# Kernel optimization log

Hardware: AMD Instinct MI355X
Metric: run time of the kernel (lower is better)

## Reference

```python
import jax, jax.numpy as jnp
import numpy as np

D_MODEL = 1024
N_HEADS = 16
SCALES = (1, 2, 4, 8)
B, S = 4, 2048
NS = len(SCALES)
E = D_MODEL // NS        # per-scale embed dim = 256
H = N_HEADS // NS        # per-scale heads = 4
DK = E // H              # head dim = 64


def setup_inputs() -> dict:
    key = jax.random.key(0)
    ks = jax.random.split(key, 6)
    sc = lambda fan_in: 1.0 / np.sqrt(fan_in)
    return {
        "x": jax.random.normal(ks[0], (B, S, D_MODEL), jnp.float32),
        # per-scale projection Linear(d_model -> E), stacked over scales
        "proj_W": jax.random.normal(ks[1], (NS, D_MODEL, E), jnp.float32) * sc(D_MODEL),
        "proj_b": jnp.zeros((NS, E), jnp.float32),
        # per-scale MultiheadAttention in_proj (q,k,v packed) and out_proj
        "in_W": jax.random.normal(ks[2], (NS, E, 3 * E), jnp.float32) * sc(E),
        "in_b": jnp.zeros((NS, 3 * E), jnp.float32),
        "out_W": jax.random.normal(ks[3], (NS, E, E), jnp.float32) * sc(E),
        "out_b": jnp.zeros((NS, E), jnp.float32),
        # fusion: Linear(d_model -> d_model) + LayerNorm (dropout is identity in eval)
        "fus_W": jax.random.normal(ks[4], (D_MODEL, D_MODEL), jnp.float32) * sc(D_MODEL),
        "fus_b": jnp.zeros((D_MODEL,), jnp.float32),
        "ln_g": jnp.ones((D_MODEL,), jnp.float32),
        "ln_b": jnp.zeros((D_MODEL,), jnp.float32),
    }


def _mha(x, in_W, in_b, out_W, out_b):
    # torch nn.MultiheadAttention, batch_first, eval mode, need_weights=True
    b, L, _ = x.shape
    qkv = x @ in_W + in_b                       # [b, L, 3E]
    q, k, v = jnp.split(qkv, 3, axis=-1)
    heads = lambda t: t.reshape(b, L, H, DK).transpose(0, 2, 1, 3)  # [b,h,L,dk]
    q, k, v = heads(q), heads(k), heads(v)
    scores = jnp.einsum('bhqd,bhkd->bhqk', q, k) / np.sqrt(DK).astype(np.float32)
    probs = jax.nn.softmax(scores, axis=-1)
    o = jnp.einsum('bhqk,bhkd->bhqd', probs, v).transpose(0, 2, 1, 3).reshape(b, L, E)
    return o @ out_W + out_b, probs.mean(axis=1)  # averaged over heads: [b,L,L]


def _upsample(y, s):
    # Faithful vectorization of the torch interpolation loop when S % s == 0:
    # full[k*s + j] = (1 - j/s)*y[k] + (j/s)*y[k+1], with zero right-neighbor
    # for the last block (torch reads attn_out_full[S-1] while it is still 0).
    if s == 1:
        return y
    b, K, d = y.shape
    y_next = jnp.concatenate([y[:, 1:], jnp.zeros_like(y[:, :1])], axis=1)
    alpha = (jnp.arange(s, dtype=y.dtype) / s)[None, None, :, None]  # [1,1,s,1]
    full = (1.0 - alpha) * y[:, :, None, :] + alpha * y_next[:, :, None, :]
    return full.reshape(b, K * s, d)


def reference(x, proj_W, proj_b, in_W, in_b, out_W, out_b, fus_W, fus_b, ln_g, ln_b):
    scale_outputs = []
    w0 = None
    for i, s in enumerate(SCALES):
        x_scale = x @ proj_W[i] + proj_b[i]        # [B,S,E]
        x_sub = x_scale[:, ::s, :]                 # strided subsequence [B,S//s,E]
        y, w = _mha(x_sub, in_W[i], in_b[i], out_W[i], out_b[i])
        scale_outputs.append(_upsample(y, s))
        if i == 0:
            w0 = w                                  # combined_weights = first scale's weights
    z = jnp.concatenate(scale_outputs, axis=-1) @ fus_W + fus_b
    mu = z.mean(-1, keepdims=True)
    var = z.var(-1, keepdims=True)
    fused = (z - mu) / jnp.sqrt(var + 1e-5) * ln_g + ln_b
    return fused, w0
```

## Files before the change

### kernel.cpp

```cpp
#include <hip/hip_runtime.h>
#include <hip/hip_bf16.h>


typedef short bh8 __attribute__((ext_vector_type(8)));
typedef float f32x4 __attribute__((ext_vector_type(4)));

#define CLOG2E 0.18033688011112042f

__device__ __forceinline__ ushort f2b(float f) {
    __hip_bfloat16 h = __float2bfloat16(f);
    return *reinterpret_cast<ushort*>(&h);
}
__device__ __forceinline__ float b2f(ushort u) {
    __hip_bfloat16 h;
    *reinterpret_cast<ushort*>(&h) = u;
    return __bfloat162float(h);
}
__device__ __forceinline__ float fexp2(float x) {
    float r;
    asm("v_exp_f32 %0, %1" : "=v"(r) : "v"(x));
    return r;
}
template<int CTRL>
__device__ __forceinline__ float dpp_mv(float x) {
    int i = __float_as_int(x);
    int r = __builtin_amdgcn_update_dpp(i, i, CTRL, 0xF, 0xF, false);
    return __int_as_float(r);
}
__device__ __forceinline__ float row_max16(float t) {
    t = fmaxf(t, dpp_mv<0x128>(t));
    t = fmaxf(t, dpp_mv<0x124>(t));
    t = fmaxf(t, dpp_mv<0x122>(t));
    t = fmaxf(t, dpp_mv<0x121>(t));
    return t;
}
__device__ __forceinline__ float row_sum16(float t) {
    t += dpp_mv<0x128>(t);
    t += dpp_mv<0x124>(t);
    t += dpp_mv<0x122>(t);
    t += dpp_mv<0x121>(t);
    return t;
}

__global__ __launch_bounds__(256) void cvt_kernel(
    const float* __restrict__ s, ushort* __restrict__ d, long n)
{
    long i = ((long)blockIdx.x * 256 + threadIdx.x) * 4;
    if (i >= n) return;
    float4 v = *(const float4*)(s + i);
    ushort4 o;
    o.x = f2b(v.x); o.y = f2b(v.y); o.z = f2b(v.z); o.w = f2b(v.w);
    *(ushort4*)(d + i) = o;
}

__global__ __launch_bounds__(256) void wtrans_kernel(
    const float* __restrict__ src, ushort* __restrict__ dst, int K, int N)
{
    __shared__ float Ls[32][33];
    const int n0 = blockIdx.x * 32, k0 = blockIdx.y * 32;
    const float* s = src + (long)blockIdx.z * K * N;
    ushort* d = dst + (long)blockIdx.z * N * K;
    const int tid = threadIdx.x;
    #pragma unroll
    for (int it = 0; it < 4; ++it) {
        int f = tid + it * 256;
        int kc = f >> 5, rn = f & 31;
        Ls[kc][rn] = s[(long)(k0 + kc) * N + n0 + rn];
    }
    __syncthreads();
    #pragma unroll
    for (int it = 0; it < 2; ++it) {
        int f = tid + it * 256;
        int rn = f >> 4, kc2 = (f & 15) * 2;
        ushort2 o;
        o.x = f2b(Ls[kc2][rn]);
        o.y = f2b(Ls[kc2 + 1][rn]);
        *(ushort2*)&d[(long)(n0 + rn) * K + k0 + kc2] = o;
    }
}

template<int MODE>
__global__ __launch_bounds__(256) void gemm_ms(
    const ushort* __restrict__ A, const ushort* __restrict__ Wt,
    const float* __restrict__ bias, ushort* __restrict__ C)
{
    constexpr int K = (MODE == 0) ? 1024 : 256;
    constexpr int N = (MODE == 1) ? 768 : 256;
    __shared__ ushort As[128][72];
    __shared__ ushort Bs[128][72];

    const int tid = threadIdx.x;
    const int wave = tid >> 6, lane = tid & 63;
    const int lm = lane & 15, quad = lane >> 4;
    const int wm = (wave & 1) * 64, wn = (wave >> 1) * 64;
    const int m0 = blockIdx.x * 128, n0 = blockIdx.y * 128;
    const int s = (m0 >= 14336) ? 3 : ((m0 >= 12288) ? 2 : ((m0 >= 8192) ? 1 : 0));
    const ushort* Wp = Wt + (long)s * N * K;
    const float* bp_ = bias + s * N;

    f32x4 acc[4][4];
    #pragma unroll
    for (int i = 0; i < 4; ++i)
        #pragma unroll
        for (int j = 0; j < 4; ++j) {
            f32x4 zz = {0.f, 0.f, 0.f, 0.f};
            acc[i][j] = zz;
        }

    const int r0 = tid >> 3, k8 = (tid & 7) * 8;
    const ushort* ap[4];
    #pragma unroll
    for (int it = 0; it < 4; ++it) {
        int m = m0 + r0 + it * 32;
        if (MODE == 0) {
            int t = m - (16384 - (16384 >> s));
            int b = t >> (11 - s);
            int tt = t - (b << (11 - s));
            ap[it] = A + ((long)(b * 2048) + ((long)tt << s)) * 1024 + k8;
        } else {
            ap[it] = A + (long)m * K + k8;
        }
    }
    const ushort* bp[4];
    #pragma unroll
    for (int it = 0; it < 4; ++it)
        bp[it] = Wp + (long)(n0 + r0 + it * 32) * K + k8;

    for (int k0 = 0; k0 < K; k0 += 64) {
        #pragma unroll
        for (int it = 0; it < 4; ++it)
            *(bh8*)&As[r0 + it * 32][k8] = *(const bh8*)(ap[it] + k0);
        #pragma unroll
        for (int it = 0; it < 4; ++it)
            *(bh8*)&Bs[r0 + it * 32][k8] = *(const bh8*)(bp[it] + k0);
        __syncthreads();
        #pragma unroll
        for (int ks = 0; ks < 2; ++ks) {
            bh8 af[4], bfv[4];
            #pragma unroll
            for (int i = 0; i < 4; ++i)
                af[i] = *(const bh8*)&As[wm + i * 16 + lm][ks * 32 + quad * 8];
            #pragma unroll
            for (int j = 0; j < 4; ++j)
                bfv[j] = *(const bh8*)&Bs[wn + j * 16 + lm][ks * 32 + quad * 8];
            #pragma unroll
            for (int i = 0; i < 4; ++i)
                #pragma unroll
                for (int j = 0; j < 4; ++j)
                    acc[i][j] = __builtin_amdgcn_mfma_f32_16x16x32_bf16(
                        af[i], bfv[j], acc[i][j], 0, 0, 0);
        }
        __syncthreads();
    }

    float bv[4]; int cols[4];
    #pragma unroll
    for (int j = 0; j < 4; ++j) {
        cols[j] = n0 + wn + j * 16 + lm;
        bv[j] = bp_[cols[j]];
    }
    #pragma unroll
    for (int i = 0; i < 4; ++i) {
        int mb = m0 + wm + i * 16 + quad * 4;
        #pragma unroll
        for (int j = 0; j < 4; ++j)
            #pragma unroll
            for (int r = 0; r < 4; ++r)
                C[(long)(mb + r) * N + cols[j]] = f2b(acc[i][j][r] + bv[j]);
    }
}

__global__ __launch_bounds__(256) void vtrans_ms(
    const ushort* __restrict__ qkvb, ushort* __restrict__ vTb)
{
    __shared__ ushort Ls[64][72];
    const int bid = blockIdx.x;
    const int s = (bid >= 896) ? 3 : ((bid >= 768) ? 2 : ((bid >= 512) ? 1 : 0));
    const int rel = bid - ((s == 0) ? 0 : ((s == 1) ? 512 : ((s == 2) ? 768 : 896)));
    const int L = 2048 >> s;
    const int z = rel >> (5 - s);
    const int kt = rel & ((32 >> s) - 1);
    const int b = z >> 2, h = z & 3;
    const ushort* src = qkvb + (long)(16384 - (16384 >> s)) * 768
                        + (long)b * L * 768 + 512 + h * 64;
    const int k0 = kt * 64;
    const int tid = threadIdx.x;
    const int kk = tid >> 3, d8 = (tid & 7) * 8;
    #pragma unroll
    for (int it = 0; it < 2; ++it) {
        int k = kk + it * 32;
        bh8 v = *(const bh8*)(src + (long)(k0 + k) * 768 + d8);
        ushort tmp[8];
        *(bh8*)tmp = v;
        #pragma unroll
        for (int j = 0; j < 8; ++j) Ls[d8 + j][k] = tmp[j];
    }
    __syncthreads();
    ushort* dst = vTb + (long)(4096 - (4096 >> s)) * 1024 + (long)z * 64 * L;
    #pragma unroll
    for (int it = 0; it < 2; ++it) {
        int d = kk + it * 32;
        *(bh8*)(dst + (long)d * L + k0 + d8) = *(const bh8*)&Ls[d][d8];
    }
}

__global__ __launch_bounds__(256, 3) void attn_ms(
    const ushort* __restrict__ qkvb, const ushort* __restrict__ vTb,
    ushort* __restrict__ ob, float* __restrict__ msc, float* __restrict__ invl)
{
    __shared__ ushort Ks[128 * 72];
    __shared__ ushort Vs[64 * 136];
    __shared__ ushort Ps[64 * 136];

    const int bid = blockIdx.x;
    const int s = (bid >= 896) ? 3 : ((bid >= 768) ? 2 : ((bid >= 512) ? 1 : 0));
    const int rel = bid - ((s == 0) ? 0 : ((s == 1) ? 512 : ((s == 2) ? 768 : 896)));
    const int L = 2048 >> s;
    const int z = rel >> (5 - s);
    const int qt = rel & ((32 >> s) - 1);
    const int b = z >> 2, h = z & 3;
    const int Rr16 = 16384 - (16384 >> s);
    const ushort* qbase = qkvb + (long)Rr16 * 768 + (long)b * L * 768 + h * 64;
    const ushort* kbase = qbase + 256;
    const ushort* vbase = vTb + (long)(4096 - (4096 >> s)) * 1024 + (long)z * 64 * L;
    ushort* o = ob + (long)Rr16 * 256;

    const int tid = threadIdx.x;
    const int wave = tid >> 6, lane = tid & 63;
    const int lm = lane & 15, quad = lane >> 4;
    const int wm = wave * 16;
    const int q0 = qt * 64;
    const int r0 = tid >> 3, k8 = (tid & 7) * 8;
    const int vd0 = tid >> 4, vc8 = (tid & 15) * 8;

    #pragma unroll
    for (int it = 0; it < 2; ++it) {
        int row = r0 + it * 32;
        *(bh8*)&Ps[row * 136 + k8] = *(const bh8*)(qbase + (long)(q0 + row) * 768 + k8);
    }
    bh8 kreg[4], vreg[4];
    #pragma unroll
    for (int it = 0; it < 4; ++it)
        kreg[it] = *(const bh8*)(kbase + (long)(r0 + it * 32) * 768 + k8);
    #pragma unroll
    for (int it = 0; it < 4; ++it)
        vreg[it] = *(const bh8*)(vbase + (long)(vd0 + it * 16) * L + vc8);
    #pragma unroll
    for (int it = 0; it < 4; ++it)
        *(bh8*)&Ks[(r0 + it * 32) * 72 + k8] = kreg[it];
    #pragma unroll
    for (int it = 0; it < 4; ++it)
        *(bh8*)&Vs[(vd0 + it * 16) * 136 + vc8] = vreg[it];
    __syncthreads();

    bh8 qf[2];
    #pragma unroll
    for (int ks = 0; ks < 2; ++ks)
        qf[ks] = *(const bh8*)&Ps[(wm + lm) * 136 + ks * 32 + quad * 8];

    f32x4 oc[4];
    #pragma unroll
    for (int nj = 0; nj < 4; ++nj) {
        f32x4 zz = {0.f, 0.f, 0.f, 0.f};
        oc[nj] = zz;
    }
    float mh[4], l_run[4];
    #pragma unroll
    for (int rr = 0; rr < 4; ++rr) { mh[rr] = -3.0e38f; l_run[rr] = 0.f; }

    for (int k0 = 0; k0 < L; k0 += 128) {
        const int kn = k0 + 128;
        const bool hasnext = kn < L;
        if (hasnext) {
            #pragma unroll
            for (int it = 0; it < 4; ++it)
                kreg[it] = *(const bh8*)(kbase + (long)(kn + r0 + it * 32) * 768 + k8);
            #pragma unroll
            for (int it = 0; it < 4; ++it)
                vreg[it] = *(const bh8*)(vbase + (long)(vd0 + it * 16) * L + kn + vc8);
        }

        f32x4 sc[8];
        #pragma unroll
        for (int nj = 0; nj < 8; ++nj) {
            f32x4 zz = {0.f, 0.f, 0.f, 0.f};
            sc[nj] = zz;
        }
        __builtin_amdgcn_s_setprio(1);
        #pragma unroll
        for (int ks = 0; ks < 2; ++ks)
            #pragma unroll
            for (int nj = 0; nj < 8; ++nj) {
                bh8 kf = *(const bh8*)&Ks[(nj * 16 + lm) * 72 + ks * 32 + quad * 8];
                sc[nj] = __builtin_amdgcn_mfma_f32_16x16x32_bf16(qf[ks], kf, sc[nj], 0, 0, 0);
            }
        __builtin_amdgcn_s_setprio(0);

        #pragma unroll
        for (int rr = 0; rr < 4; ++rr) {
            float t01 = fmaxf(sc[0][rr], sc[1][rr]);
            float t23 = fmaxf(sc[2][rr], sc[3][rr]);
            float t45 = fmaxf(sc[4][rr], sc[5][rr]);
            float t67 = fmaxf(sc[6][rr], sc[7][rr]);
            float t = fmaxf(fmaxf(t01, t23), fmaxf(t45, t67));
            t = row_max16(t);
            float mo = mh[rr];
            float mn = fmaxf(mo, t * CLOG2E);
            float alpha = fexp2(mo - mn);
            mh[rr] = mn;
            int prow = (wm + quad * 4 + rr) * 136;
            float p[8];
            #pragma unroll
            for (int nj = 0; nj < 8; ++nj) {
                p[nj] = fexp2(fmaf(sc[nj][rr], CLOG2E, -mn));
                Ps[prow + nj * 16 + lm] = f2b(p[nj]);
            }
            float rs = ((p[0] + p[1]) + (p[2] + p[3])) + ((p[4] + p[5]) + (p[6] + p[7]));
            rs = row_sum16(rs);
            l_run[rr] = l_run[rr] * alpha + rs;
            #pragma unroll
            for (int nj = 0; nj < 4; ++nj) oc[nj][rr] *= alpha;
        }

        __builtin_amdgcn_s_setprio(1);
        #pragma unroll
        for (int kst = 0; kst < 4; ++kst) {
            bh8 pf = *(const bh8*)&Ps[(wm + lm) * 136 + kst * 32 + quad * 8];
            #pragma unroll
            for (int nj = 0; nj < 4; ++nj) {
                bh8 vf = *(const bh8*)&Vs[(nj * 16 + lm) * 136 + kst * 32 + quad * 8];
                oc[nj] = __builtin_amdgcn_mfma_f32_16x16x32_bf16(pf, vf, oc[nj], 0, 0, 0);
            }
        }
        __builtin_amdgcn_s_setprio(0);

        __syncthreads();
        if (hasnext) {
            #pragma unroll
            for (int it = 0; it < 4; ++it)
                *(bh8*)&Ks[(r0 + it * 32) * 72 + k8] = kreg[it];
            #pragma unroll
            for (int it = 0; it < 4; ++it)
                *(bh8*)&Vs[(vd0 + it * 16) * 136 + vc8] = vreg[it];
            __syncthreads();
        }
    }

    #pragma unroll
    for (int rr = 0; rr < 4; ++rr) {
        float il = 1.f / l_run[rr];
        int q = q0 + wm + quad * 4 + rr;
        if (s == 0 && lm == 0) {
            msc[z * 2048 + q] = mh[rr];
            invl[z * 2048 + q] = il;
        }
        long rbase = ((long)(b * L + q)) * 256 + h * 64;
        #pragma unroll
        for (int nj = 0; nj < 4; ++nj)
            o[rbase + nj * 16 + lm] = f2b(oc[nj][rr] * il);
    }
}

__global__ __launch_bounds__(256, 2) void w0_recompute(
    const ushort* __restrict__ qkv,
    const float* __restrict__ msc, const float* __restrict__ invl,
    float* __restrict__ w0)
{
    const int L = 2048;
    __shared__ ushort SH[18432];
    ushort* Qs = SH;
    ushort* Ks = SH + 9216;
    ushort* Ws = SH;

    const int tid = threadIdx.x;
    const int wave = tid >> 6, lane = tid & 63;
    const int lm = lane & 15, quad = lane >> 4;
    const int wm = wave * 32;
    const int q0 = blockIdx.x * 128, k0 = blockIdx.y * 128;
    const int b = blockIdx.z;
    const int r0 = tid >> 3, k8 = (tid & 7) * 8;

    f32x4 acc[2][8];
    #pragma unroll
    for (int mi = 0; mi < 2; ++mi)
        #pragma unroll
        for (int nj = 0; nj < 8; ++nj) {
            f32x4 zz = {0.f, 0.f, 0.f, 0.f};
            acc[mi][nj] = zz;
        }

    for (int h = 0; h < 4; ++h) {
        const ushort* qb = qkv + (long)b * L * 768 + h * 64;
        const ushort* kb = qb + 256;
        #pragma unroll
        for (int it = 0; it < 4; ++it) {
            int r = r0 + it * 32;
            *(bh8*)&Qs[r * 72 + k8] = *(const bh8*)(qb + (long)(q0 + r) * 768 + k8);
            *(bh8*)&Ks[r * 72 + k8] = *(const bh8*)(kb + (long)(k0 + r) * 768 + k8);
        }
        __syncthreads();
        bh8 qf[2][2];
        #pragma unroll
        for (int mi = 0; mi < 2; ++mi)
            #pragma unroll
            for (int ks = 0; ks < 2; ++ks)
                qf[mi][ks] = *(const bh8*)&Qs[(wm + mi * 16 + lm) * 72 + ks * 32 + quad * 8];
        f32x4 sc[2][8];
        #pragma unroll
        for (int mi = 0; mi < 2; ++mi)
            #pragma unroll
            for (int nj = 0; nj < 8; ++nj) {
                f32x4 zz = {0.f, 0.f, 0.f, 0.f};
                sc[mi][nj] = zz;
            }
        #pragma unroll
        for (int ks = 0; ks < 2; ++ks)
            #pragma unroll
            for (int nj = 0; nj < 8; ++nj) {
                bh8 kf = *(const bh8*)&Ks[(nj * 16 + lm) * 72 + ks * 32 + quad * 8];
                #pragma unroll
                for (int mi = 0; mi < 2; ++mi)
                    sc[mi][nj] = __builtin_amdgcn_mfma_f32_16x16x32_bf16(
                        qf[mi][ks], kf, sc[mi][nj], 0, 0, 0);
            }
        const float* mz = msc + (long)(b * 4 + h) * L;
        const float* iz = invl + (long)(b * 4 + h) * L;
        #pragma unroll
        for (int mi = 0; mi < 2; ++mi)
            #pragma unroll
            for (int rr = 0; rr < 4; ++rr) {
                int q = q0 + wm + mi * 16 + quad * 4 + rr;
                float mv = mz[q], iv = iz[q];
                #pragma unroll
                for (int nj = 0; nj < 8; ++nj)
                    acc[mi][nj][rr] += fexp2(fmaf(sc[mi][nj][rr], CLOG2E, -mv)) * iv;
            }
        __syncthreads();
    }

    #pragma unroll
    for (int mi = 0; mi < 2; ++mi)
        #pragma unroll
        for (int rr = 0; rr < 4; ++rr) {
            int prow = (wm + mi * 16 + quad * 4 + rr) * 136;
            #pragma unroll
            for (int nj = 0; nj < 8; ++nj)
                Ws[prow + nj * 16 + lm] = f2b(0.25f * acc[mi][nj][rr]);
        }
    __syncthreads();
    #pragma unroll
    for (int it = 0; it < 8; ++it) {
        int idx = tid + it * 256;
        int row = idx >> 4, c8 = (idx & 15) * 8;
        ushort tmp[8];
        *(bh8*)tmp = *(const bh8*)&Ws[row * 136 + c8];
        long base = ((long)b * 2048 + q0 + row) * 2048 + k0 + c8;
        float4 f0, f1;
        f0.x = b2f(tmp[0]); f0.y = b2f(tmp[1]); f0.z = b2f(tmp[2]); f0.w = b2f(tmp[3]);
        f1.x = b2f(tmp[4]); f1.y = b2f(tmp[5]); f1.z = b2f(tmp[6]); f1.w = b2f(tmp[7]);
        *(float4*)&w0[base] = f0;
        *(float4*)&w0[base + 4] = f1;
    }
}

__global__ __launch_bounds__(256) void upsample_ms(
    const ushort* __restrict__ yallb, ushort* __restrict__ ccat)
{
    const int bid = blockIdx.x;
    const int s = bid >> 11;
    const int idx = (bid & 2047) * 256 + threadIdx.x;
    const int c4 = (idx & 63) * 4;
    const int t = (idx >> 6) & 2047;
    const int b = idx >> 17;
    const int L = 2048 >> s;
    const int k = t >> s, j = t & ((1 << s) - 1);
    const float a = (float)j / (float)(1 << s);
    const ushort* y = yallb + (long)(16384 - (16384 >> s)) * 256;
    const ushort* y0p = y + ((long)(b * L + k)) * 256 + c4;
    ushort4 y0 = *(const ushort4*)y0p;
    ushort4 y1 = {0, 0, 0, 0};
    if (k + 1 < L) y1 = *(const ushort4*)(y0p + 256);
    ushort4 o;
    o.x = f2b((1.f - a) * b2f(y0.x) + a * b2f(y1.x));
    o.y = f2b((1.f - a) * b2f(y0.y) + a * b2f(y1.y));
    o.z = f2b((1.f - a) * b2f(y0.z) + a * b2f(y1.z));
    o.w = f2b((1.f - a) * b2f(y0.w) + a * b2f(y1.w));
    *(ushort4*)&ccat[((long)(b * 2048 + t)) * 1024 + s * 256 + c4] = o;
}

__global__ __launch_bounds__(256) void gemm_fus(
    const ushort* __restrict__ A, const ushort* __restrict__ Wt,
    const float* __restrict__ bias, float* __restrict__ C)
{
    const int K = 1024, N = 1024;
    __shared__ ushort As[128][72];
    __shared__ ushort Bs[128][72];
    const int tid = threadIdx.x;
    const int wave = tid >> 6, lane = tid & 63;
    const int lm = lane & 15, quad = lane >> 4;
    const int wm = (wave & 1) * 64, wn = (wave >> 1) * 64;
    const int m0 = blockIdx.x * 128, n0 = blockIdx.y * 128;

    f32x4 acc[4][4];
    #pragma unroll
    for (int i = 0; i < 4; ++i)
        #pragma unroll
        for (int j = 0; j < 4; ++j) {
            f32x4 zz = {0.f, 0.f, 0.f, 0.f};
            acc[i][j] = zz;
        }
    const int r0 = tid >> 3, k8 = (tid & 7) * 8;
    for (int k0 = 0; k0 < K; k0 += 64) {
        #pragma unroll
        for (int it = 0; it < 4; ++it) {
            int r = r0 + it * 32;
            *(bh8*)&As[r][k8] = *(const bh8*)(A + (long)(m0 + r) * K + k0 + k8);
            *(bh8*)&Bs[r][k8] = *(const bh8*)(Wt + (long)(n0 + r) * K + k0 + k8);
        }
        __syncthreads();
        #pragma unroll
        for (int ks = 0; ks < 2; ++ks) {
            bh8 af[4], bfv[4];
            #pragma unroll
            for (int i = 0; i < 4; ++i)
                af[i] = *(const bh8*)&As[wm + i * 16 + lm][ks * 32 + quad * 8];
            #pragma unroll
            for (int j = 0; j < 4; ++j)
                bfv[j] = *(const bh8*)&Bs[wn + j * 16 + lm][ks * 32 + quad * 8];
            #pragma unroll
            for (int i = 0; i < 4; ++i)
                #pragma unroll
                for (int j = 0; j < 4; ++j)
                    acc[i][j] = __builtin_amdgcn_mfma_f32_16x16x32_bf16(
                        af[i], bfv[j], acc[i][j], 0, 0, 0);
        }
        __syncthreads();
    }
    float bv[4]; int cols[4];
    #pragma unroll
    for (int j = 0; j < 4; ++j) {
        cols[j] = n0 + wn + j * 16 + lm;
        bv[j] = bias[cols[j]];
    }
    #pragma unroll
    for (int i = 0; i < 4; ++i) {
        int mb = m0 + wm + i * 16 + quad * 4;
        #pragma unroll
        for (int j = 0; j < 4; ++j)
            #pragma unroll
            for (int r = 0; r < 4; ++r)
                C[(long)(mb + r) * N + cols[j]] = acc[i][j][r] + bv[j];
    }
}

__global__ __launch_bounds__(256) void ln_kernel(
    float* __restrict__ zbuf, const float* __restrict__ g, const float* __restrict__ bta)
{
    long row = blockIdx.x;
    float* p = zbuf + row * 1024;
    const int tid = threadIdx.x;
    float4 v = *(const float4*)(p + tid * 4);
    float s = (v.x + v.y) + (v.z + v.w);
    #pragma unroll
    for (int off = 32; off; off >>= 1) s += __shfl_xor(s, off);
    __shared__ float r0[4], r1[4];
    int wid = tid >> 6;
    if ((tid & 63) == 0) r0[wid] = s;
    __syncthreads();
    s = r0[0] + r0[1] + r0[2] + r0[3];
    float mu = s * (1.f / 1024.f);
    float dx = v.x - mu, dy = v.y - mu, dz = v.z - mu, dw = v.w - mu;
    float q = (dx * dx + dy * dy) + (dz * dz + dw * dw);
    #pragma unroll
    for (int off = 32; off; off >>= 1) q += __shfl_xor(q, off);
    if ((tid & 63) == 0) r1[wid] = q;
    __syncthreads();
    q = r1[0] + r1[1] + r1[2] + r1[3];
    float rstd = rsqrtf(q * (1.f / 1024.f) + 1e-5f);
    float4 gg = *(const float4*)(g + tid * 4);
    float4 bb = *(const float4*)(bta + tid * 4);
    float4 o;
    o.x = dx * rstd * gg.x + bb.x;
    o.y = dy * rstd * gg.y + bb.y;
    o.z = dz * rstd * gg.z + bb.z;
    o.w = dw * rstd * gg.w + bb.w;
    *(float4*)(p + tid * 4) = o;
}

extern "C" void kernel_launch(void* const* d_in, const int* in_sizes, int n_in,
                              void* d_out, int out_size, void* d_ws, size_t ws_size,
                              hipStream_t stream)
{
    const float* x     = (const float*)d_in[0];
    const float* projW = (const float*)d_in[1];
    const float* projB = (const float*)d_in[2];
    const float* inW   = (const float*)d_in[3];
    const float* inB   = (const float*)d_in[4];
    const float* outW  = (const float*)d_in[5];
    const float* outB  = (const float*)d_in[6];
    const float* fusW  = (const float*)d_in[7];
    const float* fusB  = (const float*)d_in[8];
    const float* lnG   = (const float*)d_in[9];
    const float* lnB   = (const float*)d_in[10];

    float* fused  = (float*)d_out;
    float* out_w0 = fused + 8388608;

    char* w = (char*)d_ws;
    ushort* xb     = (ushort*)w; w += 16777216;
    ushort* pT     = (ushort*)w; w += 2097152;
    ushort* iT     = (ushort*)w; w += 1572864;
    ushort* oT     = (ushort*)w; w += 524288;
    ushort* fT     = (ushort*)w; w += 2097152;
    ushort* xprojb = (ushort*)w; w += 7864320;
    ushort* qkvb   = (ushort*)w; w += 23592960;
    ushort* ob     = (ushort*)w; w += 7864320;
    ushort* yallb  = (ushort*)w; w += 7864320;
    ushort* ccatb  = (ushort*)w; w += 16777216;
    ushort* vTb    = (ushort*)w; w += 7864320;
    float*  msc    = (float*)w;  w += 131072;
    float*  invl   = (float*)w;  w += 131072;

    cvt_kernel<<<8192, 256, 0, stream>>>(x, xb, 8388608);
    wtrans_kernel<<<dim3(8, 32, 4), 256, 0, stream>>>(projW, pT, 1024, 256);
    wtrans_kernel<<<dim3(24, 8, 4), 256, 0, stream>>>(inW, iT, 256, 768);
    wtrans_kernel<<<dim3(8, 8, 4), 256, 0, stream>>>(outW, oT, 256, 256);
    wtrans_kernel<<<dim3(32, 32, 1), 256, 0, stream>>>(fusW, fT, 1024, 1024);

    gemm_ms<0><<<dim3(120, 2), 256, 0, stream>>>(xb, pT, projB, xprojb);
    gemm_ms<1><<<dim3(120, 6), 256, 0, stream>>>(xprojb, iT, inB, qkvb);
    vtrans_ms<<<960, 256, 0, stream>>>(qkvb, vTb);
    attn_ms<<<960, 256, 0, stream>>>(qkvb, vTb, ob, msc, invl);
    w0_recompute<<<dim3(16, 16, 4), 256, 0, stream>>>(qkvb, msc, invl, out_w0);
    gemm_ms<2><<<dim3(120, 2), 256, 0, stream>>>(ob, oT, outB, yallb);
    upsample_ms<<<8192, 256, 0, stream>>>(yallb, ccatb);
    gemm_fus<<<dim3(64, 8), 256, 0, stream>>>(ccatb, fT, fusB, fused);
    ln_kernel<<<8192, 256, 0, stream>>>(fused, lnG, lnB);
}
```

Baseline: 340.1 us.

## Fuse prep kernels, prefetch GEMM tiles into registers, shrink BM for small GEMMs

Merges the input-convert and four weight-transpose launches into one prep kernel to cut launch overhead. Adds register prefetch of the next K-tile in the GEMMs, fusion GEMM and the w0 recompute Q/K loads, so global loads overlap MFMA work, and raises wave priority around MFMA blocks. Halves the M tile to 64 for the projection and out-proj GEMMs, doubling grid size to fill more CUs. This costs more registers, an extra barrier per iteration, and more B-tile reloads in the smaller-tile GEMMs.

```diff
diff --git a/kernel.cpp b/kernel.cpp
--- a/kernel.cpp
+++ b/kernel.cpp
@@ -42,25 +42,13 @@
     return t;
 }
 
-__global__ __launch_bounds__(256) void cvt_kernel(
-    const float* __restrict__ s, ushort* __restrict__ d, long n)
-{
-    long i = ((long)blockIdx.x * 256 + threadIdx.x) * 4;
-    if (i >= n) return;
-    float4 v = *(const float4*)(s + i);
-    ushort4 o;
-    o.x = f2b(v.x); o.y = f2b(v.y); o.z = f2b(v.z); o.w = f2b(v.w);
-    *(ushort4*)(d + i) = o;
-}
-
-__global__ __launch_bounds__(256) void wtrans_kernel(
-    const float* __restrict__ src, ushort* __restrict__ dst, int K, int N)
-{
-    __shared__ float Ls[32][33];
-    const int n0 = blockIdx.x * 32, k0 = blockIdx.y * 32;
-    const float* s = src + (long)blockIdx.z * K * N;
-    ushort* d = dst + (long)blockIdx.z * N * K;
-    const int tid = threadIdx.x;
+__device__ __forceinline__ void wtrans_body(
+    const float* __restrict__ src, ushort* __restrict__ dst,
+    int K, int N, int bx, int by, int z, int tid, float (*Ls)[33])
+{
+    const int n0 = bx * 32, k0 = by * 32;
+    const float* s = src + (long)z * K * N;
+    ushort* d = dst + (long)z * N * K;
     #pragma unroll
     for (int it = 0; it < 4; ++it) {
         int f = tid + it * 256;
@@ -79,6 +67,40 @@
     }
 }
 
+__global__ __launch_bounds__(256) void prep_kernel(
+    const float* __restrict__ x, ushort* __restrict__ xb,
+    const float* __restrict__ projW, ushort* __restrict__ pT,
+    const float* __restrict__ inW, ushort* __restrict__ iT,
+    const float* __restrict__ outW, ushort* __restrict__ oT,
+    const float* __restrict__ fusW, ushort* __restrict__ fT)
+{
+    __shared__ float Ls[32][33];
+    const int bid = blockIdx.x;
+    const int tid = threadIdx.x;
+    if (bid < 8192) {
+        long i = ((long)bid * 256 + tid) * 4;
+        float4 v = *(const float4*)(x + i);
+        ushort4 o;
+        o.x = f2b(v.x); o.y = f2b(v.y); o.z = f2b(v.z); o.w = f2b(v.w);
+        *(ushort4*)(xb + i) = o;
+    } else if (bid < 9216) {
+        int rel = bid - 8192;
+        int z = rel >> 8, rem = rel & 255;
+        wtrans_body(projW, pT, 1024, 256, rem & 7, rem >> 3, z, tid, Ls);
+    } else if (bid < 9984) {
+        int rel = bid - 9216;
+        int z = rel / 192, rem = rel - z * 192;
+        wtrans_body(inW, iT, 256, 768, rem % 24, rem / 24, z, tid, Ls);
+    } else if (bid < 10240) {
+        int rel = bid - 9984;
+        int z = rel >> 6, rem = rel & 63;
+        wtrans_body(outW, oT, 256, 256, rem & 7, rem >> 3, z, tid, Ls);
+    } else {
+        int rel = bid - 10240;
+        wtrans_body(fusW, fT, 1024, 1024, rel & 31, rel >> 5, 0, tid, Ls);
+    }
+}
+
 template<int MODE>
 __global__ __launch_bounds__(256) void gemm_ms(
     const ushort* __restrict__ A, const ushort* __restrict__ Wt,
@@ -86,21 +108,24 @@
 {
     constexpr int K = (MODE == 0) ? 1024 : 256;
     constexpr int N = (MODE == 1) ? 768 : 256;
-    __shared__ ushort As[128][72];
+    constexpr int BM = (MODE == 1) ? 128 : 64;
+    constexpr int MF = BM / 32;
+    constexpr int AITS = BM / 32;
+    __shared__ ushort As[BM][72];
     __shared__ ushort Bs[128][72];
 
     const int tid = threadIdx.x;
     const int wave = tid >> 6, lane = tid & 63;
     const int lm = lane & 15, quad = lane >> 4;
-    const int wm = (wave & 1) * 64, wn = (wave >> 1) * 64;
-    const int m0 = blockIdx.x * 128, n0 = blockIdx.y * 128;
+    const int wm = (wave & 1) * (BM / 2), wn = (wave >> 1) * 64;
+    const int m0 = blockIdx.x * BM, n0 = blockIdx.y * 128;
     const int s = (m0 >= 14336) ? 3 : ((m0 >= 12288) ? 2 : ((m0 >= 8192) ? 1 : 0));
     const ushort* Wp = Wt + (long)s * N * K;
     const float* bp_ = bias + s * N;
 
-    f32x4 acc[4][4];
-    #pragma unroll
-    for (int i = 0; i < 4; ++i)
+    f32x4 acc[MF][4];
+    #pragma unroll
+    for (int i = 0; i < MF; ++i)
         #pragma unroll
         for (int j = 0; j < 4; ++j) {
             f32x4 zz = {0.f, 0.f, 0.f, 0.f};
@@ -108,9 +133,9 @@
         }
 
     const int r0 = tid >> 3, k8 = (tid & 7) * 8;
-    const ushort* ap[4];
-    #pragma unroll
-    for (int it = 0; it < 4; ++it) {
+    const ushort* ap[AITS];
+    #pragma unroll
+    for (int it = 0; it < AITS; ++it) {
         int m = m0 + r0 + it * 32;
         if (MODE == 0) {
             int t = m - (16384 - (16384 >> s));
@@ -126,31 +151,52 @@
     for (int it = 0; it < 4; ++it)
         bp[it] = Wp + (long)(n0 + r0 + it * 32) * K + k8;
 
+    bh8 areg[AITS], breg[4];
+    #pragma unroll
+    for (int it = 0; it < AITS; ++it) areg[it] = *(const bh8*)(ap[it]);
+    #pragma unroll
+    for (int it = 0; it < 4; ++it) breg[it] = *(const bh8*)(bp[it]);
+    #pragma unroll
+    for (int it = 0; it < AITS; ++it) *(bh8*)&As[r0 + it * 32][k8] = areg[it];
+    #pragma unroll
+    for (int it = 0; it < 4; ++it) *(bh8*)&Bs[r0 + it * 32][k8] = breg[it];
+    __syncthreads();
+
     for (int k0 = 0; k0 < K; k0 += 64) {
-        #pragma unroll
-        for (int it = 0; it < 4; ++it)
-            *(bh8*)&As[r0 + it * 32][k8] = *(const bh8*)(ap[it] + k0);
-        #pragma unroll
-        for (int it = 0; it < 4; ++it)
-            *(bh8*)&Bs[r0 + it * 32][k8] = *(const bh8*)(bp[it] + k0);
-        __syncthreads();
+        const int kn = k0 + 64;
+        const bool hasnext = kn < K;
+        if (hasnext) {
+            #pragma unroll
+            for (int it = 0; it < AITS; ++it) areg[it] = *(const bh8*)(ap[it] + kn);
+            #pragma unroll
+            for (int it = 0; it < 4; ++it) breg[it] = *(const bh8*)(bp[it] + kn);
+        }
+        __builtin_amdgcn_s_setprio(1);
         #pragma unroll
         for (int ks = 0; ks < 2; ++ks) {
-            bh8 af[4], bfv[4];
-            #pragma unroll
-            for (int i = 0; i < 4; ++i)
+            bh8 af[MF], bfv[4];
+            #pragma unroll
+            for (int i = 0; i < MF; ++i)
                 af[i] = *(const bh8*)&As[wm + i * 16 + lm][ks * 32 + quad * 8];
             #pragma unroll
             for (int j = 0; j < 4; ++j)
                 bfv[j] = *(const bh8*)&Bs[wn + j * 16 + lm][ks * 32 + quad * 8];
             #pragma unroll
-            for (int i = 0; i < 4; ++i)
+            for (int i = 0; i < MF; ++i)
                 #pragma unroll
                 for (int j = 0; j < 4; ++j)
                     acc[i][j] = __builtin_amdgcn_mfma_f32_16x16x32_bf16(
                         af[i], bfv[j], acc[i][j], 0, 0, 0);
         }
+        __builtin_amdgcn_s_setprio(0);
         __syncthreads();
+        if (hasnext) {
+            #pragma unroll
+            for (int it = 0; it < AITS; ++it) *(bh8*)&As[r0 + it * 32][k8] = areg[it];
+            #pragma unroll
+            for (int it = 0; it < 4; ++it) *(bh8*)&Bs[r0 + it * 32][k8] = breg[it];
+            __syncthreads();
+        }
     }
 
     float bv[4]; int cols[4];
@@ -160,7 +206,7 @@
         bv[j] = bp_[cols[j]];
     }
     #pragma unroll
-    for (int i = 0; i < 4; ++i) {
+    for (int i = 0; i < MF; ++i) {
         int mb = m0 + wm + i * 16 + quad * 4;
         #pragma unroll
         for (int j = 0; j < 4; ++j)
@@ -389,16 +435,36 @@
             acc[mi][nj] = zz;
         }
 
-    for (int h = 0; h < 4; ++h) {
-        const ushort* qb = qkv + (long)b * L * 768 + h * 64;
+    bh8 qreg[4], kreg[4];
+    {
+        const ushort* qb = qkv + (long)b * L * 768;
         const ushort* kb = qb + 256;
         #pragma unroll
         for (int it = 0; it < 4; ++it) {
             int r = r0 + it * 32;
-            *(bh8*)&Qs[r * 72 + k8] = *(const bh8*)(qb + (long)(q0 + r) * 768 + k8);
-            *(bh8*)&Ks[r * 72 + k8] = *(const bh8*)(kb + (long)(k0 + r) * 768 + k8);
+            qreg[it] = *(const bh8*)(qb + (long)(q0 + r) * 768 + k8);
+            kreg[it] = *(const bh8*)(kb + (long)(k0 + r) * 768 + k8);
+        }
+    }
+
+    for (int h = 0; h < 4; ++h) {
+        #pragma unroll
+        for (int it = 0; it < 4; ++it) {
+            int r = r0 + it * 32;
+            *(bh8*)&Qs[r * 72 + k8] = qreg[it];
+            *(bh8*)&Ks[r * 72 + k8] = kreg[it];
         }
         __syncthreads();
+        if (h < 3) {
+            const ushort* qb = qkv + (long)b * L * 768 + (h + 1) * 64;
+            const ushort* kb = qb + 256;
+            #pragma unroll
+            for (int it = 0; it < 4; ++it) {
+                int r = r0 + it * 32;
+                qreg[it] = *(const bh8*)(qb + (long)(q0 + r) * 768 + k8);
+                kreg[it] = *(const bh8*)(kb + (long)(k0 + r) * 768 + k8);
+            }
+        }
         bh8 qf[2][2];
         #pragma unroll
         for (int mi = 0; mi < 2; ++mi)
@@ -413,6 +479,7 @@
                 f32x4 zz = {0.f, 0.f, 0.f, 0.f};
                 sc[mi][nj] = zz;
             }
+        __builtin_amdgcn_s_setprio(1);
         #pragma unroll
         for (int ks = 0; ks < 2; ++ks)
             #pragma unroll
@@ -423,6 +490,7 @@
                     sc[mi][nj] = __builtin_amdgcn_mfma_f32_16x16x32_bf16(
                         qf[mi][ks], kf, sc[mi][nj], 0, 0, 0);
             }
+        __builtin_amdgcn_s_setprio(0);
         const float* mz = msc + (long)(b * 4 + h) * L;
         const float* iz = invl + (long)(b * 4 + h) * L;
         #pragma unroll
@@ -510,14 +578,33 @@
             acc[i][j] = zz;
         }
     const int r0 = tid >> 3, k8 = (tid & 7) * 8;
+    const ushort* ap = A + (long)(m0 + r0) * K + k8;
+    const ushort* bp = Wt + (long)(n0 + r0) * K + k8;
+
+    bh8 areg[4], breg[4];
+    #pragma unroll
+    for (int it = 0; it < 4; ++it) {
+        areg[it] = *(const bh8*)(ap + (long)(it * 32) * K);
+        breg[it] = *(const bh8*)(bp + (long)(it * 32) * K);
+    }
+    #pragma unroll
+    for (int it = 0; it < 4; ++it) {
+        *(bh8*)&As[r0 + it * 32][k8] = areg[it];
+        *(bh8*)&Bs[r0 + it * 32][k8] = breg[it];
+    }
+    __syncthreads();
+
     for (int k0 = 0; k0 < K; k0 += 64) {
-        #pragma unroll
-        for (int it = 0; it < 4; ++it) {
-            int r = r0 + it * 32;
-            *(bh8*)&As[r][k8] = *(const bh8*)(A + (long)(m0 + r) * K + k0 + k8);
-            *(bh8*)&Bs[r][k8] = *(const bh8*)(Wt + (long)(n0 + r) * K + k0 + k8);
-        }
-        __syncthreads();
+        const int kn = k0 + 64;
+        const bool hasnext = kn < K;
+        if (hasnext) {
+            #pragma unroll
+            for (int it = 0; it < 4; ++it) {
+                areg[it] = *(const bh8*)(ap + (long)(it * 32) * K + kn);
+                breg[it] = *(const bh8*)(bp + (long)(it * 32) * K + kn);
+            }
+        }
+        __builtin_amdgcn_s_setprio(1);
         #pragma unroll
         for (int ks = 0; ks < 2; ++ks) {
             bh8 af[4], bfv[4];
@@ -534,7 +621,16 @@
                     acc[i][j] = __builtin_amdgcn_mfma_f32_16x16x32_bf16(
                         af[i], bfv[j], acc[i][j], 0, 0, 0);
         }
+        __builtin_amdgcn_s_setprio(0);
         __syncthreads();
+        if (hasnext) {
+            #pragma unroll
+            for (int it = 0; it < 4; ++it) {
+                *(bh8*)&As[r0 + it * 32][k8] = areg[it];
+                *(bh8*)&Bs[r0 + it * 32][k8] = breg[it];
+            }
+            __syncthreads();
+        }
     }
     float bv[4]; int cols[4];
     #pragma unroll
@@ -621,18 +717,15 @@
     float*  msc    = (float*)w;  w += 131072;
     float*  invl   = (float*)w;  w += 131072;
 
-    cvt_kernel<<<8192, 256, 0, stream>>>(x, xb, 8388608);
-    wtrans_kernel<<<dim3(8, 32, 4), 256, 0, stream>>>(projW, pT, 1024, 256);
-    wtrans_kernel<<<dim3(24, 8, 4), 256, 0, stream>>>(inW, iT, 256, 768);
-    wtrans_kernel<<<dim3(8, 8, 4), 256, 0, stream>>>(outW, oT, 256, 256);
-    wtrans_kernel<<<dim3(32, 32, 1), 256, 0, stream>>>(fusW, fT, 1024, 1024);
-
-    gemm_ms<0><<<dim3(120, 2), 256, 0, stream>>>(xb, pT, projB, xprojb);
+    prep_kernel<<<11264, 256, 0, stream>>>(x, xb, projW, pT, inW, iT,
+                                           outW, oT, fusW, fT);
+
+    gemm_ms<0><<<dim3(240, 2), 256, 0, stream>>>(xb, pT, projB, xprojb);
     gemm_ms<1><<<dim3(120, 6), 256, 0, stream>>>(xprojb, iT, inB, qkvb);
     vtrans_ms<<<960, 256, 0, stream>>>(qkvb, vTb);
     attn_ms<<<960, 256, 0, stream>>>(qkvb, vTb, ob, msc, invl);
     w0_recompute<<<dim3(16, 16, 4), 256, 0, stream>>>(qkvb, msc, invl, out_w0);
-    gemm_ms<2><<<dim3(120, 2), 256, 0, stream>>>(ob, oT, outB, yallb);
+    gemm_ms<2><<<dim3(240, 2), 256, 0, stream>>>(ob, oT, outB, yallb);
     upsample_ms<<<8192, 256, 0, stream>>>(yallb, ccatb);
     gemm_fus<<<dim3(64, 8), 256, 0, stream>>>(ccatb, fT, fusB, fused);
     ln_kernel<<<8192, 256, 0, stream>>>(fused, lnG, lnB);
```

New measurement: 318.1 us. -6.4%, faster.
